# Optimization experiments

Measured on AMD Instinct MI355X. Metric: run time of the kernel, lower is better.

## Reference

```python
import jax, jax.numpy as jnp
import numpy as np

NMS_POST = 500      # nms_post_maxsize
NMS_PRE = 4096      # nms_pre_maxsize
NMS_THRESH = 0.5
SCORE_THRESH = 0.1
NUM_BOXES = 2_000_000
NUM_CLASSES = 10


def setup_inputs() -> dict:
    key = jax.random.key(0)
    k1, k2, k3 = jax.random.split(key, 3)
    # valid axis-aligned boxes: centers in [0,100), sizes in [1,6)
    ctr = jax.random.uniform(k1, (2, NUM_BOXES), dtype=jnp.float32) * 100.0
    wh = 1.0 + jax.random.uniform(k2, (2, NUM_BOXES), dtype=jnp.float32) * 5.0
    x1y1 = ctr - 0.5 * wh
    x2y2 = ctr + 0.5 * wh
    batch_box_preds = jnp.stack([x1y1[0], x1y1[1], x2y2[0], x2y2[1]], axis=0)[None]  # (1,4,N)
    batch_cls_preds = jax.random.uniform(k3, (1, NUM_CLASSES, NUM_BOXES), dtype=jnp.float32)  # (1,C,N)
    return {"batch_box_preds": batch_box_preds, "batch_cls_preds": batch_cls_preds}


def _nms(batch_box_preds, batch_cls_preds):
    boxes = jnp.transpose(batch_box_preds[0])        # (N,4) x1,y1,x2,y2
    cls = batch_cls_preds[0]                          # (C,N)
    scores = jnp.max(cls, axis=0)                     # (N,)
    labels = jnp.argmax(cls, axis=0)                  # (N,) int

    # score threshold: invalidate low scores before top-k
    masked = jnp.where(scores >= SCORE_THRESH, scores, -1.0)
    vals, idx = jax.lax.top_k(masked, NMS_PRE)        # sorted desc
    bk = boxes[idx]                                   # (K,4)
    lk = labels[idx]                                  # (K,)
    valid = vals >= SCORE_THRESH                      # (K,)

    # pairwise IoU (K,K)
    x1, y1, x2, y2 = bk[:, 0], bk[:, 1], bk[:, 2], bk[:, 3]
    area = jnp.clip(x2 - x1, 0.0) * jnp.clip(y2 - y1, 0.0)
    iw = jnp.clip(jnp.minimum(x2[:, None], x2[None, :]) - jnp.maximum(x1[:, None], x1[None, :]), 0.0)
    ih = jnp.clip(jnp.minimum(y2[:, None], y2[None, :]) - jnp.maximum(y1[:, None], y1[None, :]), 0.0)
    inter = iw * ih
    iou = inter / (area[:, None] + area[None, :] - inter + 1e-8)

    # greedy suppression in score order
    K = NMS_PRE
    arange_k = jnp.arange(K)

    def body(keep, i):
        sup = keep[i] & (iou[i] > NMS_THRESH) & (arange_k > i)
        return keep & ~sup, None

    keep, _ = jax.lax.scan(body, valid, arange_k)

    final_scores = jnp.where(keep, vals, -1.0)
    sv, si = jax.lax.top_k(final_scores, NMS_POST)    # top post kept boxes (score order)
    ob = bk[si]                                       # (P,4)
    ol = lk[si]                                       # (P,)
    m = sv >= SCORE_THRESH                            # pad mask
    out = jnp.concatenate(
        [
            jnp.where(m[:, None], ob, 0.0),
            jnp.where(m, sv, 0.0)[:, None],
            jnp.where(m, ol, 0).astype(jnp.float32)[:, None],
        ],
        axis=1,
    )
    return out[None]  # (1, NMS_POST, 6): x1,y1,x2,y2,score,label


def reference(batch_box_preds, batch_cls_preds):
    return _nms(batch_box_preds, batch_cls_preds)
```

## Files before the change

kernel.cpp:

```cpp
#include <hip/hip_runtime.h>
#include <stdint.h>

#define NBOX 2000000
#define NCLS 10
#define KPRE 4096
#define KPOST 500
#define GCAP 6144
#define NMW  (GCAP / 64)
#define PCAP 131072
#define LPC  16384
#define PROWS (GCAP / 64)
#define BSEL 4096

#define OFF_KEYS  ((size_t)0)
#define OFF_PAIRS ((size_t)8000000)
#define OFF_ARR   (OFF_PAIRS + (size_t)PCAP * 4)
#define OFF_LAB   (OFF_ARR + (size_t)GCAP * 32)
#define OFF_ZERO  (OFF_LAB + (size_t)NBOX)
#define ZW_HIST0  0
#define ZW_HIST2  256
#define ZW_HIST16 512
#define ZW_STATE  (512 + 65536)
#define ZERO_WORDS (ZW_STATE + 16)
#define ZERO_BYTES ((size_t)ZERO_WORDS * 4)

#define HOTBASE 0x4080u

__device__ __forceinline__ uint32_t f2ord(float f) {
  uint32_t b = __float_as_uint(f);
  return (b & 0x80000000u) ? ~b : (b | 0x80000000u);
}
__device__ __forceinline__ float ord2f(uint32_t ord) {
  uint32_t b = (ord & 0x80000000u) ? (ord ^ 0x80000000u) : ~ord;
  return __uint_as_float(b);
}

__device__ __forceinline__ unsigned long long shflx64(unsigned long long v, int mask) {
  union { unsigned long long u; int i[2]; } a; a.u = v;
  a.i[0] = __shfl_xor(a.i[0], mask, 64);
  a.i[1] = __shfl_xor(a.i[1], mask, 64);
  return a.u;
}

__device__ __forceinline__ void wave_bucket(const uint32_t* __restrict__ h, uint32_t need,
                                            uint32_t* bin_out, uint32_t* nd_out) {
  int l = threadIdx.x & 63;
  uint4 h4 = reinterpret_cast<const uint4*>(h)[l];
  uint32_t s = h4.x + h4.y + h4.z + h4.w;
  uint32_t p = s;
  #pragma unroll
  for (int d = 1; d < 64; d <<= 1) {
    uint32_t v = __shfl_up(p, d, 64);
    if (l >= d) p += v;
  }
  uint32_t e0 = p - s, e1 = e0 + h4.x, e2 = e1 + h4.y, e3 = e2 + h4.z, e4 = e3 + h4.w;
  uint32_t eb[5] = {e0, e1, e2, e3, e4};
  uint32_t bin = 0xFFFFFFFFu, nd = 1;
  #pragma unroll
  for (int q = 0; q < 4; ++q)
    if (eb[q] < need && need <= eb[q + 1]) { bin = (uint32_t)(4 * l + q); nd = need - eb[q]; }
  unsigned long long mm = __ballot(bin != 0xFFFFFFFFu);
  int src = mm ? __builtin_ctzll(mm) : 0;
  *bin_out = (uint32_t)__shfl((int)bin, src);
  *nd_out  = (uint32_t)__shfl((int)nd, src);
}

__device__ __forceinline__ void wave_compact32(bool take, uint32_t key,
                                               uint32_t* counter, uint32_t* buf,
                                               uint32_t cap) {
  unsigned long long mm = __ballot(take);
  if (take) {
    int lane = threadIdx.x & 63;
    unsigned long long lt = (lane == 0) ? 0ull : (~0ull >> (64 - lane));
    int rank = __builtin_popcountll(mm & lt);
    int leader = __builtin_ctzll(mm);
    uint32_t base = 0;
    if (rank == 0) base = atomicAdd(counter, (uint32_t)__builtin_popcountll(mm));
    base = __shfl(base, leader);
    uint32_t pos = base + (uint32_t)rank;
    if (pos < cap) buf[pos] = key;
  }
}

__device__ __forceinline__ void tree10(float v0, float v1, float v2, float v3, float v4,
                                       float v5, float v6, float v7, float v8, float v9,
                                       float* mv, int* mi) {
  float b0, b1, b2, b3, b4; int j0, j1, j2, j3, j4;
  if (v1 > v0) { b0 = v1; j0 = 1; } else { b0 = v0; j0 = 0; }
  if (v3 > v2) { b1 = v3; j1 = 3; } else { b1 = v2; j1 = 2; }
  if (v5 > v4) { b2 = v5; j2 = 5; } else { b2 = v4; j2 = 4; }
  if (v7 > v6) { b3 = v7; j3 = 7; } else { b3 = v6; j3 = 6; }
  if (v9 > v8) { b4 = v9; j4 = 9; } else { b4 = v8; j4 = 8; }
  if (b1 > b0) { b0 = b1; j0 = j1; }
  if (b3 > b2) { b2 = b3; j2 = j3; }
  if (b2 > b0) { b0 = b2; j0 = j2; }
  if (b4 > b0) { b0 = b4; j0 = j4; }
  *mv = b0; *mi = j0;
}


__global__ void k_score(const float* __restrict__ cls, uint32_t* __restrict__ keys,
                        uint8_t* __restrict__ labs, uint32_t* __restrict__ hist0,
                        uint32_t* __restrict__ hist16) {
  __shared__ uint32_t lh0[256];
  __shared__ uint32_t lhr[128];
  for (int i = threadIdx.x; i < 256; i += blockDim.x) lh0[i] = 0;
  for (int i = threadIdx.x; i < 128; i += blockDim.x) lhr[i] = 0;
  __syncthreads();
  const int nvec = NBOX / 4;
  const float4* cp = reinterpret_cast<const float4*>(cls);
  const int pstr = NBOX / 4;
  for (int v = blockIdx.x * blockDim.x + threadIdx.x; v < nvec; v += gridDim.x * blockDim.x) {
    float4 x0 = cp[v];
    float4 x1 = cp[pstr * 1 + v];
    float4 x2 = cp[pstr * 2 + v];
    float4 x3 = cp[pstr * 3 + v];
    float4 x4 = cp[pstr * 4 + v];
    float4 x5 = cp[pstr * 5 + v];
    float4 x6 = cp[pstr * 6 + v];
    float4 x7 = cp[pstr * 7 + v];
    float4 x8 = cp[pstr * 8 + v];
    float4 x9 = cp[pstr * 9 + v];
    uint32_t u4[4]; int l4[4];
    float mv; int mi;
    tree10(x0.x, x1.x, x2.x, x3.x, x4.x, x5.x, x6.x, x7.x, x8.x, x9.x, &mv, &mi);
    { float ms = (mv >= 0.1f) ? mv : -1.0f; u4[0] = ~f2ord(ms); l4[0] = mi; }
    tree10(x0.y, x1.y, x2.y, x3.y, x4.y, x5.y, x6.y, x7.y, x8.y, x9.y, &mv, &mi);
    { float ms = (mv >= 0.1f) ? mv : -1.0f; u4[1] = ~f2ord(ms); l4[1] = mi; }
    tree10(x0.z, x1.z, x2.z, x3.z, x4.z, x5.z, x6.z, x7.z, x8.z, x9.z, &mv, &mi);
    { float ms = (mv >= 0.1f) ? mv : -1.0f; u4[2] = ~f2ord(ms); l4[2] = mi; }
    tree10(x0.w, x1.w, x2.w, x3.w, x4.w, x5.w, x6.w, x7.w, x8.w, x9.w, &mv, &mi);
    { float ms = (mv >= 0.1f) ? mv : -1.0f; u4[3] = ~f2ord(ms); l4[3] = mi; }
    #pragma unroll
    for (int q = 0; q < 4; ++q) {
      uint32_t b16 = u4[q] >> 16;
      uint32_t rel = b16 - HOTBASE;
      if (rel < 128u) atomicAdd(&lhr[rel], 1u);
      else { atomicAdd(&hist16[b16], 1u); atomicAdd(&lh0[b16 >> 8], 1u); }
    }
    reinterpret_cast<uint4*>(keys)[v] = make_uint4(u4[0], u4[1], u4[2], u4[3]);
    uchar4 lb; lb.x = (uint8_t)l4[0]; lb.y = (uint8_t)l4[1];
    lb.z = (uint8_t)l4[2]; lb.w = (uint8_t)l4[3];
    reinterpret_cast<uchar4*>(labs)[v] = lb;
  }
  __syncthreads();
  for (int i = threadIdx.x; i < 128; i += blockDim.x) {
    uint32_t c = lhr[i];
    if (c) { atomicAdd(&hist16[HOTBASE + i], c); atomicAdd(&lh0[HOTBASE >> 8], c); }
  }
  __syncthreads();
  for (int i = threadIdx.x; i < 256; i += blockDim.x)
    if (lh0[i]) atomicAdd(&hist0[i], lh0[i]);
}

__global__ void k_hist2(const uint32_t* __restrict__ keys,
                        const uint32_t* __restrict__ hist0,
                        const uint32_t* __restrict__ hist16,
                        uint32_t* __restrict__ hist2,
                        float* __restrict__ x1a, float* __restrict__ y1a,
                        float* __restrict__ x2a, float* __restrict__ y2a,
                        float* __restrict__ vala, int* __restrict__ laba,
                        unsigned long long* __restrict__ skg) {
  __shared__ uint32_t lh[256];
  __shared__ uint32_t sp16;
  if (threadIdx.x < 64) {
    uint32_t b1, nd1, b2, nd2;
    wave_bucket(hist0, KPRE, &b1, &nd1);
    wave_bucket(hist16 + ((size_t)b1 << 8), nd1, &b2, &nd2);
    if (threadIdx.x == 0) sp16 = (b1 << 8) | b2;
  }
  for (int i = threadIdx.x; i < 256; i += blockDim.x) lh[i] = 0;
  __syncthreads();
  uint32_t p16 = sp16;
  const int nvec = NBOX / 4;
  int gtid = blockIdx.x * blockDim.x + threadIdx.x;
  int gtot = gridDim.x * blockDim.x;
  for (int v = gtid; v < nvec; v += gtot) {
    uint4 kv = reinterpret_cast<const uint4*>(keys)[v];
    if ((kv.x >> 16) == p16) atomicAdd(&lh[(kv.x >> 8) & 255u], 1u);
    if ((kv.y >> 16) == p16) atomicAdd(&lh[(kv.y >> 8) & 255u], 1u);
    if ((kv.z >> 16) == p16) atomicAdd(&lh[(kv.z >> 8) & 255u], 1u);
    if ((kv.w >> 16) == p16) atomicAdd(&lh[(kv.w >> 8) & 255u], 1u);
  }
  for (int t = gtid; t < GCAP; t += gtot) {
    x1a[t] = 0.0f; y1a[t] = 0.0f; x2a[t] = 0.0f; y2a[t] = 0.0f;
    vala[t] = -1.0f; laba[t] = 0; skg[t] = ~0ull;
  }
  __syncthreads();
  for (int i = threadIdx.x; i < 256; i += blockDim.x)
    if (lh[i]) atomicAdd(&hist2[i], lh[i]);
}

__global__ void k_selgather(const uint32_t* __restrict__ keys,
                            const float* __restrict__ boxes, const uint8_t* __restrict__ labs,
                            const uint32_t* __restrict__ hist0,
                            const uint32_t* __restrict__ hist16,
                            const uint32_t* __restrict__ hist2,
                            uint32_t* __restrict__ selcnt,
                            float* __restrict__ x1a, float* __restrict__ y1a,
                            float* __restrict__ x2a, float* __restrict__ y2a,
                            float* __restrict__ vala, int* __restrict__ laba,
                            unsigned long long* __restrict__ skg) {
  __shared__ uint32_t sp24, bcnt, bbase;
  __shared__ uint32_t lu[BSEL];
  __shared__ uint32_t li[BSEL];
  if (threadIdx.x < 64) {
    uint32_t b1, nd1, b2, nd2, b3, nd3;
    wave_bucket(hist0, KPRE, &b1, &nd1);
    wave_bucket(hist16 + ((size_t)b1 << 8), nd1, &b2, &nd2);
    wave_bucket(hist2, nd2, &b3, &nd3);
    if (threadIdx.x == 0) sp24 = (((b1 << 8) | b2) << 8) | b3;
  }
  if (threadIdx.x == 0) bcnt = 0;
  __syncthreads();
  uint32_t p24 = sp24;
  const int nvec = NBOX / 4;
  for (int v = blockIdx.x * blockDim.x + threadIdx.x; v < nvec; v += gridDim.x * blockDim.x) {
    uint4 kv = reinterpret_cast<const uint4*>(keys)[v];
    uint32_t us[4] = {kv.x, kv.y, kv.z, kv.w};
    #pragma unroll
    for (int q = 0; q < 4; ++q) {
      uint32_t u = us[q];
      if ((u >> 8) <= p24) {
        uint32_t p = atomicAdd(&bcnt, 1u);
        if (p < (uint32_t)BSEL) { lu[p] = u; li[p] = (uint32_t)(4 * v + q); }
      }
    }
  }
  __syncthreads();
  if (threadIdx.x == 0) {
    uint32_t c = bcnt; if (c > (uint32_t)BSEL) c = (uint32_t)BSEL;
    bbase = c ? atomicAdd(selcnt, c) : 0u;
    bcnt = c;
  }
  __syncthreads();
  uint32_t c = bcnt, base = bbase;
  for (uint32_t i = threadIdx.x; i < c; i += blockDim.x) {
    uint32_t pos = base + i;
    if (pos < (uint32_t)GCAP) {
      uint32_t idx = li[i];
      uint32_t u = lu[i];
      x1a[pos] = boxes[idx];
      y1a[pos] = boxes[(size_t)NBOX + idx];
      x2a[pos] = boxes[(size_t)2 * NBOX + idx];
      y2a[pos] = boxes[(size_t)3 * NBOX + idx];
      vala[pos] = ord2f(~u);
      laba[pos] = (int)labs[idx];
      skg[pos] = ((unsigned long long)u << 32) | idx;
    }
  }
}

__global__ void k_pairs(const float* __restrict__ x1a, const float* __restrict__ y1a,
                        const float* __restrict__ x2a, const float* __restrict__ y2a,
                        const unsigned long long* __restrict__ skg,
                        uint32_t* __restrict__ paircnt, uint32_t* __restrict__ pairs) {
#pragma clang fp contract(off)
  int bx = blockIdx.x, by = blockIdx.y;
  if (bx < by) return;
  int t = threadIdx.x;
  int i = by * 64 + t;
  __shared__ float sx1[64], sy1[64], sx2[64], sy2[64], sar[64];
  __shared__ unsigned long long sk[64];
  int j0 = bx * 64 + t;
  float cx1 = x1a[j0], cy1 = y1a[j0], cx2 = x2a[j0], cy2 = y2a[j0];
  sx1[t] = cx1; sy1[t] = cy1; sx2[t] = cx2; sy2[t] = cy2;
  sar[t] = fmaxf(cx2 - cx1, 0.0f) * fmaxf(cy2 - cy1, 0.0f);
  sk[t] = skg[j0];
  __syncthreads();
  float x1i = x1a[i], y1i = y1a[i], x2i = x2a[i], y2i = y2a[i];
  unsigned long long rk = skg[i];
  float ari = fmaxf(x2i - x1i, 0.0f) * fmaxf(y2i - y1i, 0.0f);
  unsigned long long w = 0ull;
  #pragma unroll 8
  for (int jj = 0; jj < 64; ++jj) {
    int j = bx * 64 + jj;
    float iw = fmaxf(fminf(x2i, sx2[jj]) - fmaxf(x1i, sx1[jj]), 0.0f);
    float ih = fmaxf(fminf(y2i, sy2[jj]) - fmaxf(y1i, sy1[jj]), 0.0f);
    float inter = iw * ih;
    float den = ((ari + sar[jj]) - inter) + 1e-8f;
    float iou = inter / den;
    if ((iou > 0.5f) && (j > i)) w |= (1ull << jj);
  }
  while (__ballot(w != 0ull)) {
    bool tk = (w != 0ull);
    uint32_t pr = 0;
    if (tk) {
      int b = __builtin_ctzll(w); w &= w - 1;
      int j = bx * 64 + b;
      bool i_sup = (rk < sk[b]);
      pr = i_sup ? (((uint32_t)i << 16) | (uint32_t)j)
                 : (((uint32_t)j << 16) | (uint32_t)i);
    }
    wave_compact32(tk, pr, paircnt, pairs, (uint32_t)PCAP);
  }
}

__global__ void __launch_bounds__(1024) k_fix(
    const uint32_t* __restrict__ state, const uint32_t* __restrict__ pairs,
    const float* __restrict__ x1a, const float* __restrict__ y1a,
    const float* __restrict__ x2a, const float* __restrict__ y2a,
    const float* __restrict__ vala, const int* __restrict__ laba,
    const unsigned long long* __restrict__ skg, float* __restrict__ out) {
  __shared__ unsigned long long lk[GCAP];
  __shared__ uint32_t lpair[LPC];
  __shared__ unsigned long long validm[NMW], accm[NMW];
  __shared__ uint32_t supp[NMW * 2];
  __shared__ uint32_t hsel[256];
  __shared__ uint32_t lsel[512];
  __shared__ unsigned long long kkbuf[512];
  __shared__ uint32_t chg, scnt2, sneedS;
  __shared__ unsigned long long spre;
  __shared__ uint32_t orlo, orhi, andlo, andhi;
  int tid = threadIdx.x;
  int lane = tid & 63;

  uint32_t gc = state[0]; if (gc > (uint32_t)GCAP) gc = (uint32_t)GCAP;
  uint32_t np = state[1]; if (np > (uint32_t)PCAP) np = (uint32_t)PCAP;
  for (int t = tid; t < KPOST * 6; t += 1024) out[t] = 0.0f;
  if (tid < 512) kkbuf[tid] = ~0ull;
  for (int t = tid; t < GCAP; t += 1024) lk[t] = (t < (int)gc) ? skg[t] : ~0ull;
  bool plds = (np <= (uint32_t)LPC);
  if (plds) for (uint32_t p = (uint32_t)tid; p < np; p += 1024) lpair[p] = pairs[p];
  if (tid == 0) { orlo = 0; orhi = 0; andlo = ~0u; andhi = ~0u; scnt2 = 0; }
  __syncthreads();

  uint32_t need1 = (gc < (uint32_t)KPRE) ? gc : (uint32_t)KPRE;
  if (need1 == 0) return;
  {
    unsigned long long myor = 0ull, myand = ~0ull;
    for (int t = tid; t < (int)gc; t += 1024) {
      unsigned long long k = lk[t];
      myor |= k; myand &= k;
    }
    #pragma unroll
    for (int d = 1; d < 64; d <<= 1) { myor |= shflx64(myor, d); myand &= shflx64(myand, d); }
    if (lane == 0) {
      atomicOr(&orlo, (uint32_t)myor); atomicOr(&orhi, (uint32_t)(myor >> 32));
      atomicAnd(&andlo, (uint32_t)myand); atomicAnd(&andhi, (uint32_t)(myand >> 32));
    }
  }
  __syncthreads();
  unsigned long long T1;
  {
    unsigned long long vor = ((unsigned long long)orhi << 32) | orlo;
    unsigned long long vand = ((unsigned long long)andhi << 32) | andlo;
    unsigned long long diff = vor ^ vand;
    unsigned long long pre = 0;
    uint32_t need = need1;
    for (int b = 7; b >= 0; --b) {
      uint32_t db = (uint32_t)(diff >> (8 * b)) & 255u;
      if (db == 0) { pre = (pre << 8) | ((uint32_t)(vand >> (8 * b)) & 255u); continue; }
      if (tid < 256) hsel[tid] = 0;
      __syncthreads();
      for (int t = tid; t < (int)gc; t += 1024) {
        unsigned long long k = lk[t];
        bool pm = (b == 7) ? true : ((k >> (8 * b + 8)) == pre);
        if (pm) atomicAdd(&hsel[(uint32_t)(k >> (8 * b)) & 255u], 1u);
      }
      __syncthreads();
      if (tid < 64) {
        uint32_t c0 = hsel[4 * tid], c1 = hsel[4 * tid + 1],
                 c2 = hsel[4 * tid + 2], c3 = hsel[4 * tid + 3];
        uint32_t s = c0 + c1 + c2 + c3;
        uint32_t p = s;
        #pragma unroll
        for (int d = 1; d < 64; d <<= 1) {
          uint32_t v = __shfl_up(p, d, 64);
          if (tid >= d) p += v;
        }
        uint32_t e0 = p - s, e1 = e0 + c0, e2 = e1 + c1, e3 = e2 + c2, e4 = e3 + c3;
        uint32_t eb[5] = {e0, e1, e2, e3, e4};
        #pragma unroll
        for (int q = 0; q < 4; ++q)
          if (eb[q] < need && need <= eb[q + 1]) {
            spre = (pre << 8) | (uint32_t)(4 * tid + q);
            sneedS = need - eb[q];
          }
      }
      __syncthreads();
      pre = spre; need = sneedS;
      __syncthreads();
    }
    T1 = pre;
  }

  for (int t = tid; t < GCAP; t += 1024) {
    unsigned long long k = lk[t];
    float v = ord2f(~(uint32_t)(k >> 32));
    bool ok = (k <= T1) && (v >= 0.1f);
    unsigned long long bm = __ballot(ok);
    if (lane == 0) { validm[t >> 6] = bm; accm[t >> 6] = bm; }
  }
  __syncthreads();

  while (true) {
    __syncthreads();
    if (tid < NMW * 2) supp[tid] = 0;
    if (tid == 0) chg = 0;
    __syncthreads();
    if (plds) {
      for (uint32_t p = (uint32_t)tid; p < np; p += 1024) {
        uint32_t pr = lpair[p];
        uint32_t i = pr >> 16, j = pr & 0xffffu;
        if ((accm[i >> 6] >> (i & 63)) & 1ull) atomicOr(&supp[j >> 5], 1u << (j & 31));
      }
    } else {
      for (uint32_t p = (uint32_t)tid; p < np; p += 1024) {
        uint32_t pr = pairs[p];
        uint32_t i = pr >> 16, j = pr & 0xffffu;
        if ((accm[i >> 6] >> (i & 63)) & 1ull) atomicOr(&supp[j >> 5], 1u << (j & 31));
      }
    }
    __syncthreads();
    if (tid < NMW) {
      unsigned long long s = ((unsigned long long)supp[2 * tid + 1] << 32) | supp[2 * tid];
      unsigned long long na = validm[tid] & ~s;
      if (na != accm[tid]) { accm[tid] = na; atomicOr(&chg, 1u); }
    }
    __syncthreads();
    if (chg == 0) break;
  }

  if (tid == 0) {
    uint32_t ns = 0;
    for (int l = 0; l < NMW; ++l) ns += (uint32_t)__builtin_popcountll(accm[l]);
    sneedS = (ns < (uint32_t)KPOST) ? ns : (uint32_t)KPOST;
    orlo = 0; orhi = 0; andlo = ~0u; andhi = ~0u;
  }
  __syncthreads();
  uint32_t need0 = sneedS;
  if (need0 == 0) return;
  {
    unsigned long long myor = 0ull, myand = ~0ull;
    for (int t = tid; t < GCAP; t += 1024) {
      if ((accm[t >> 6] >> (t & 63)) & 1ull) {
        unsigned long long k = lk[t];
        myor |= k; myand &= k;
      }
    }
    #pragma unroll
    for (int d = 1; d < 64; d <<= 1) { myor |= shflx64(myor, d); myand &= shflx64(myand, d); }
    if (lane == 0) {
      atomicOr(&orlo, (uint32_t)myor); atomicOr(&orhi, (uint32_t)(myor >> 32));
      atomicAnd(&andlo, (uint32_t)myand); atomicAnd(&andhi, (uint32_t)(myand >> 32));
    }
  }
  __syncthreads();
  unsigned long long T2;
  {
    unsigned long long vor = ((unsigned long long)orhi << 32) | orlo;
    unsigned long long vand = ((unsigned long long)andhi << 32) | andlo;
    unsigned long long diff = vor ^ vand;
    unsigned long long pre = 0;
    uint32_t need = need0;
    for (int b = 7; b >= 0; --b) {
      uint32_t db = (uint32_t)(diff >> (8 * b)) & 255u;
      if (db == 0) { pre = (pre << 8) | ((uint32_t)(vand >> (8 * b)) & 255u); continue; }
      if (tid < 256) hsel[tid] = 0;
      __syncthreads();
      for (int t = tid; t < GCAP; t += 1024) {
        if ((accm[t >> 6] >> (t & 63)) & 1ull) {
          unsigned long long k = lk[t];
          bool pm = (b == 7) ? true : ((k >> (8 * b + 8)) == pre);
          if (pm) atomicAdd(&hsel[(uint32_t)(k >> (8 * b)) & 255u], 1u);
        }
      }
      __syncthreads();
      if (tid < 64) {
        uint32_t c0 = hsel[4 * tid], c1 = hsel[4 * tid + 1],
                 c2 = hsel[4 * tid + 2], c3 = hsel[4 * tid + 3];
        uint32_t s = c0 + c1 + c2 + c3;
        uint32_t p = s;
        #pragma unroll
        for (int d = 1; d < 64; d <<= 1) {
          uint32_t v = __shfl_up(p, d, 64);
          if (tid >= d) p += v;
        }
        uint32_t e0 = p - s, e1 = e0 + c0, e2 = e1 + c1, e3 = e2 + c2, e4 = e3 + c3;
        uint32_t eb[5] = {e0, e1, e2, e3, e4};
        #pragma unroll
        for (int q = 0; q < 4; ++q)
          if (eb[q] < need && need <= eb[q + 1]) {
            spre = (pre << 8) | (uint32_t)(4 * tid + q);
            sneedS = need - eb[q];
          }
      }
      __syncthreads();
      pre = spre; need = sneedS;
      __syncthreads();
    }
    T2 = pre;
  }

  for (int t = tid; t < GCAP; t += 1024) {
    bool take = ((accm[t >> 6] >> (t & 63)) & 1ull) && (lk[t] <= T2);
    wave_compact32(take, (uint32_t)t, &scnt2, lsel, 512u);
  }
  __syncthreads();
  uint32_t cnt = min(scnt2, 512u);
  if (tid < (int)cnt) kkbuf[tid] = lk[lsel[tid]];
  __syncthreads();
  if (tid < (int)cnt) {
    unsigned long long k0 = kkbuf[tid];
    uint32_t rank = 0;
    #pragma unroll 8
    for (uint32_t p = 0; p < 512u; ++p) rank += (kkbuf[p] < k0) ? 1u : 0u;
    if (rank < (uint32_t)KPOST) {
      int i = (int)lsel[tid];
      out[rank * 6 + 0] = x1a[i];
      out[rank * 6 + 1] = y1a[i];
      out[rank * 6 + 2] = x2a[i];
      out[rank * 6 + 3] = y2a[i];
      out[rank * 6 + 4] = vala[i];
      out[rank * 6 + 5] = (float)laba[i];
    }
  }
}

extern "C" void kernel_launch(void* const* d_in, const int* in_sizes, int n_in,
                              void* d_out, int out_size, void* d_ws, size_t ws_size,
                              hipStream_t stream) {
  const float* boxes = (const float*)d_in[0];
  const float* cls   = (const float*)d_in[1];
  float* out = (float*)d_out;
  char* ws = (char*)d_ws;

  uint32_t* keys = (uint32_t*)(ws + OFF_KEYS);
  uint32_t* pairs = (uint32_t*)(ws + OFF_PAIRS);
  float* x1a = (float*)(ws + OFF_ARR);
  float* y1a = x1a + GCAP;
  float* x2a = y1a + GCAP;
  float* y2a = x2a + GCAP;
  float* vala = y2a + GCAP;
  int* laba = (int*)(vala + GCAP);
  unsigned long long* skg = (unsigned long long*)(laba + GCAP);
  uint8_t* labs = (uint8_t*)(ws + OFF_LAB);
  uint32_t* zbase = (uint32_t*)(ws + OFF_ZERO);
  uint32_t* hist0 = zbase + ZW_HIST0;
  uint32_t* hist2 = zbase + ZW_HIST2;
  uint32_t* hist16 = zbase + ZW_HIST16;
  uint32_t* state = zbase + ZW_STATE;
  uint32_t* selcnt = state;
  uint32_t* paircnt = state + 1;

  hipMemsetAsync(ws + OFF_ZERO, 0, ZERO_BYTES, stream);
  k_score<<<1024, 256, 0, stream>>>(cls, keys, labs, hist0, hist16);
  k_hist2<<<512, 256, 0, stream>>>(keys, hist0, hist16, hist2,
                                   x1a, y1a, x2a, y2a, vala, laba, skg);
  k_selgather<<<512, 256, 0, stream>>>(keys, boxes, labs, hist0, hist16, hist2,
                                       selcnt, x1a, y1a, x2a, y2a, vala, laba, skg);
  k_pairs<<<dim3(PROWS, PROWS), 64, 0, stream>>>(x1a, y1a, x2a, y2a, skg, paircnt, pairs);
  k_fix<<<1, 1024, 0, stream>>>(state, pairs, x1a, y1a, x2a, y2a, vala, laba, skg, out);
}
```

Before: 223.6 us.

## Fuse hist2+selgather and pairs+fix kernels using software grid barriers

Merges the second-level histogram and selection/gather kernels into one persistent 256-block kernel that uses a flag-based grid barrier between the phases. It also merges the pairwise IoU kernel with the single-block fix-up kernel: all blocks compute triangular tiles indexed per wave, then signal block 0, which waits and runs the greedy resolution. The aim is to cut kernel launch gaps and the wasted lower-triangle blocks. The cost is spin-wait barriers that assume all 256 blocks are co-resident, plus a smaller per-block selection buffer.

```diff
diff --git a/kernel.cpp b/kernel.cpp
--- a/kernel.cpp
+++ b/kernel.cpp
@@ -9,8 +9,9 @@
 #define NMW  (GCAP / 64)
 #define PCAP 131072
 #define LPC  16384
-#define PROWS (GCAP / 64)
-#define BSEL 4096
+#define MSEL 2048
+#define NBLKM 256
+#define NWAV 16
 
 #define OFF_KEYS  ((size_t)0)
 #define OFF_PAIRS ((size_t)8000000)
@@ -21,7 +22,10 @@
 #define ZW_HIST2  256
 #define ZW_HIST16 512
 #define ZW_STATE  (512 + 65536)
-#define ZERO_WORDS (ZW_STATE + 16)
+#define SW_REL1   2
+#define SW_FLAGS1 16
+#define SW_FLAGS2 272
+#define ZERO_WORDS (ZW_STATE + 544)
 #define ZERO_BYTES ((size_t)ZERO_WORDS * 4)
 
 #define HOTBASE 0x4080u
@@ -40,6 +44,32 @@
   a.i[0] = __shfl_xor(a.i[0], mask, 64);
   a.i[1] = __shfl_xor(a.i[1], mask, 64);
   return a.u;
+}
+
+__device__ __forceinline__ void mid_bar(uint32_t* flags1, uint32_t* rel1) {
+  __syncthreads();
+  int tid = threadIdx.x;
+  if (blockIdx.x == 0) {
+    if (tid >= 1 && tid < NBLKM) {
+      while (!__hip_atomic_load(&flags1[tid], __ATOMIC_RELAXED, __HIP_MEMORY_SCOPE_AGENT))
+        __builtin_amdgcn_s_sleep(2);
+    }
+    __syncthreads();
+    if (tid == 0) {
+      __threadfence();
+      __hip_atomic_store(rel1, 1u, __ATOMIC_RELAXED, __HIP_MEMORY_SCOPE_AGENT);
+    }
+    __syncthreads();
+  } else {
+    if (tid == 0) {
+      __threadfence();
+      __hip_atomic_store(&flags1[blockIdx.x], 1u, __ATOMIC_RELAXED, __HIP_MEMORY_SCOPE_AGENT);
+      while (!__hip_atomic_load(rel1, __ATOMIC_RELAXED, __HIP_MEMORY_SCOPE_AGENT))
+        __builtin_amdgcn_s_sleep(2);
+      __threadfence();
+    }
+    __syncthreads();
+  }
 }
 
 __device__ __forceinline__ void wave_bucket(const uint32_t* __restrict__ h, uint32_t need,
@@ -153,28 +183,36 @@
     if (lh0[i]) atomicAdd(&hist0[i], lh0[i]);
 }
 
-__global__ void k_hist2(const uint32_t* __restrict__ keys,
-                        const uint32_t* __restrict__ hist0,
-                        const uint32_t* __restrict__ hist16,
-                        uint32_t* __restrict__ hist2,
-                        float* __restrict__ x1a, float* __restrict__ y1a,
-                        float* __restrict__ x2a, float* __restrict__ y2a,
-                        float* __restrict__ vala, int* __restrict__ laba,
-                        unsigned long long* __restrict__ skg) {
+__global__ void __launch_bounds__(1024) k_mid(
+    const uint32_t* __restrict__ keys,
+    const float* __restrict__ boxes, const uint8_t* __restrict__ labs,
+    const uint32_t* __restrict__ hist0, const uint32_t* __restrict__ hist16,
+    uint32_t* __restrict__ hist2, uint32_t* __restrict__ state,
+    float* __restrict__ x1a, float* __restrict__ y1a,
+    float* __restrict__ x2a, float* __restrict__ y2a,
+    float* __restrict__ vala, int* __restrict__ laba,
+    unsigned long long* __restrict__ skg) {
   __shared__ uint32_t lh[256];
-  __shared__ uint32_t sp16;
-  if (threadIdx.x < 64) {
+  __shared__ uint32_t lu[MSEL];
+  __shared__ uint32_t li[MSEL];
+  __shared__ uint32_t sp16, sp24, bcnt, bbase;
+  int tid = threadIdx.x, blk = blockIdx.x;
+  int gtid = blk * 1024 + tid;
+  const int gtot = NBLKM * 1024;
+  const int nvec = NBOX / 4;
+  uint32_t* selcnt = state;
+  uint32_t* flags1 = state + SW_FLAGS1;
+  uint32_t* rel1 = state + SW_REL1;
+
+  if (tid < 64) {
     uint32_t b1, nd1, b2, nd2;
     wave_bucket(hist0, KPRE, &b1, &nd1);
     wave_bucket(hist16 + ((size_t)b1 << 8), nd1, &b2, &nd2);
-    if (threadIdx.x == 0) sp16 = (b1 << 8) | b2;
-  }
-  for (int i = threadIdx.x; i < 256; i += blockDim.x) lh[i] = 0;
+    if (tid == 0) sp16 = (b1 << 8) | b2;
+  }
+  for (int i = tid; i < 256; i += 1024) lh[i] = 0;
   __syncthreads();
   uint32_t p16 = sp16;
-  const int nvec = NBOX / 4;
-  int gtid = blockIdx.x * blockDim.x + threadIdx.x;
-  int gtot = gridDim.x * blockDim.x;
   for (int v = gtid; v < nvec; v += gtot) {
     uint4 kv = reinterpret_cast<const uint4*>(keys)[v];
     if ((kv.x >> 16) == p16) atomicAdd(&lh[(kv.x >> 8) & 255u], 1u);
@@ -187,35 +225,22 @@
     vala[t] = -1.0f; laba[t] = 0; skg[t] = ~0ull;
   }
   __syncthreads();
-  for (int i = threadIdx.x; i < 256; i += blockDim.x)
+  for (int i = tid; i < 256; i += 1024)
     if (lh[i]) atomicAdd(&hist2[i], lh[i]);
-}
-
-__global__ void k_selgather(const uint32_t* __restrict__ keys,
-                            const float* __restrict__ boxes, const uint8_t* __restrict__ labs,
-                            const uint32_t* __restrict__ hist0,
-                            const uint32_t* __restrict__ hist16,
-                            const uint32_t* __restrict__ hist2,
-                            uint32_t* __restrict__ selcnt,
-                            float* __restrict__ x1a, float* __restrict__ y1a,
-                            float* __restrict__ x2a, float* __restrict__ y2a,
-                            float* __restrict__ vala, int* __restrict__ laba,
-                            unsigned long long* __restrict__ skg) {
-  __shared__ uint32_t sp24, bcnt, bbase;
-  __shared__ uint32_t lu[BSEL];
-  __shared__ uint32_t li[BSEL];
-  if (threadIdx.x < 64) {
+
+  mid_bar(flags1, rel1);
+
+  if (tid < 64) {
     uint32_t b1, nd1, b2, nd2, b3, nd3;
     wave_bucket(hist0, KPRE, &b1, &nd1);
     wave_bucket(hist16 + ((size_t)b1 << 8), nd1, &b2, &nd2);
     wave_bucket(hist2, nd2, &b3, &nd3);
-    if (threadIdx.x == 0) sp24 = (((b1 << 8) | b2) << 8) | b3;
-  }
-  if (threadIdx.x == 0) bcnt = 0;
+    if (tid == 0) sp24 = (((b1 << 8) | b2) << 8) | b3;
+  }
+  if (tid == 0) bcnt = 0;
   __syncthreads();
   uint32_t p24 = sp24;
-  const int nvec = NBOX / 4;
-  for (int v = blockIdx.x * blockDim.x + threadIdx.x; v < nvec; v += gridDim.x * blockDim.x) {
+  for (int v = gtid; v < nvec; v += gtot) {
     uint4 kv = reinterpret_cast<const uint4*>(keys)[v];
     uint32_t us[4] = {kv.x, kv.y, kv.z, kv.w};
     #pragma unroll
@@ -223,19 +248,19 @@
       uint32_t u = us[q];
       if ((u >> 8) <= p24) {
         uint32_t p = atomicAdd(&bcnt, 1u);
-        if (p < (uint32_t)BSEL) { lu[p] = u; li[p] = (uint32_t)(4 * v + q); }
-      }
-    }
-  }
-  __syncthreads();
-  if (threadIdx.x == 0) {
-    uint32_t c = bcnt; if (c > (uint32_t)BSEL) c = (uint32_t)BSEL;
+        if (p < (uint32_t)MSEL) { lu[p] = u; li[p] = (uint32_t)(4 * v + q); }
+      }
+    }
+  }
+  __syncthreads();
+  if (tid == 0) {
+    uint32_t c = bcnt; if (c > (uint32_t)MSEL) c = (uint32_t)MSEL;
     bbase = c ? atomicAdd(selcnt, c) : 0u;
     bcnt = c;
   }
   __syncthreads();
   uint32_t c = bcnt, base = bbase;
-  for (uint32_t i = threadIdx.x; i < c; i += blockDim.x) {
+  for (uint32_t i = (uint32_t)tid; i < c; i += 1024) {
     uint32_t pos = base + i;
     if (pos < (uint32_t)GCAP) {
       uint32_t idx = li[i];
@@ -251,57 +276,13 @@
   }
 }
 
-__global__ void k_pairs(const float* __restrict__ x1a, const float* __restrict__ y1a,
-                        const float* __restrict__ x2a, const float* __restrict__ y2a,
-                        const unsigned long long* __restrict__ skg,
-                        uint32_t* __restrict__ paircnt, uint32_t* __restrict__ pairs) {
-#pragma clang fp contract(off)
-  int bx = blockIdx.x, by = blockIdx.y;
-  if (bx < by) return;
-  int t = threadIdx.x;
-  int i = by * 64 + t;
-  __shared__ float sx1[64], sy1[64], sx2[64], sy2[64], sar[64];
-  __shared__ unsigned long long sk[64];
-  int j0 = bx * 64 + t;
-  float cx1 = x1a[j0], cy1 = y1a[j0], cx2 = x2a[j0], cy2 = y2a[j0];
-  sx1[t] = cx1; sy1[t] = cy1; sx2[t] = cx2; sy2[t] = cy2;
-  sar[t] = fmaxf(cx2 - cx1, 0.0f) * fmaxf(cy2 - cy1, 0.0f);
-  sk[t] = skg[j0];
-  __syncthreads();
-  float x1i = x1a[i], y1i = y1a[i], x2i = x2a[i], y2i = y2a[i];
-  unsigned long long rk = skg[i];
-  float ari = fmaxf(x2i - x1i, 0.0f) * fmaxf(y2i - y1i, 0.0f);
-  unsigned long long w = 0ull;
-  #pragma unroll 8
-  for (int jj = 0; jj < 64; ++jj) {
-    int j = bx * 64 + jj;
-    float iw = fmaxf(fminf(x2i, sx2[jj]) - fmaxf(x1i, sx1[jj]), 0.0f);
-    float ih = fmaxf(fminf(y2i, sy2[jj]) - fmaxf(y1i, sy1[jj]), 0.0f);
-    float inter = iw * ih;
-    float den = ((ari + sar[jj]) - inter) + 1e-8f;
-    float iou = inter / den;
-    if ((iou > 0.5f) && (j > i)) w |= (1ull << jj);
-  }
-  while (__ballot(w != 0ull)) {
-    bool tk = (w != 0ull);
-    uint32_t pr = 0;
-    if (tk) {
-      int b = __builtin_ctzll(w); w &= w - 1;
-      int j = bx * 64 + b;
-      bool i_sup = (rk < sk[b]);
-      pr = i_sup ? (((uint32_t)i << 16) | (uint32_t)j)
-                 : (((uint32_t)j << 16) | (uint32_t)i);
-    }
-    wave_compact32(tk, pr, paircnt, pairs, (uint32_t)PCAP);
-  }
-}
-
-__global__ void __launch_bounds__(1024) k_fix(
-    const uint32_t* __restrict__ state, const uint32_t* __restrict__ pairs,
+__global__ void __launch_bounds__(1024) k_tail(
+    uint32_t* __restrict__ state, uint32_t* __restrict__ pairs,
     const float* __restrict__ x1a, const float* __restrict__ y1a,
     const float* __restrict__ x2a, const float* __restrict__ y2a,
     const float* __restrict__ vala, const int* __restrict__ laba,
     const unsigned long long* __restrict__ skg, float* __restrict__ out) {
+#pragma clang fp contract(off)
   __shared__ unsigned long long lk[GCAP];
   __shared__ uint32_t lpair[LPC];
   __shared__ unsigned long long validm[NMW], accm[NMW];
@@ -312,11 +293,89 @@
   __shared__ uint32_t chg, scnt2, sneedS;
   __shared__ unsigned long long spre;
   __shared__ uint32_t orlo, orhi, andlo, andhi;
-  int tid = threadIdx.x;
-  int lane = tid & 63;
+  int tid = threadIdx.x, blk = blockIdx.x;
+  int wid = tid >> 6, lane = tid & 63;
+  uint32_t* paircnt = state + 1;
+  uint32_t* flags2 = state + SW_FLAGS2;
 
   uint32_t gc = state[0]; if (gc > (uint32_t)GCAP) gc = (uint32_t)GCAP;
-  uint32_t np = state[1]; if (np > (uint32_t)PCAP) np = (uint32_t)PCAP;
+
+  {
+    int rows = (int)((gc + 63) >> 6);
+    int NT = rows * (rows + 1) / 2;
+    float* psx1 = (float*)lpair;
+    float* psy1 = psx1 + NWAV * 64;
+    float* psx2 = psy1 + NWAV * 64;
+    float* psy2 = psx2 + NWAV * 64;
+    float* psar = psy2 + NWAV * 64;
+    unsigned long long* psk = (unsigned long long*)(psar + NWAV * 64);
+    int W = blk * NWAV + wid;
+    int wb = wid << 6;
+    for (int T = W; T < NT; T += NBLKM * NWAV) {
+      float Rf = (float)rows;
+      float disc = (2.0f * Rf + 1.0f) * (2.0f * Rf + 1.0f) - 8.0f * (float)T;
+      disc = disc > 0.0f ? disc : 0.0f;
+      int by = (int)(((2.0f * Rf + 1.0f) - sqrtf(disc)) * 0.5f);
+      if (by < 0) by = 0;
+      if (by > rows - 1) by = rows - 1;
+      while (by > 0 && T < by * rows - (by * (by - 1)) / 2) --by;
+      while (by < rows - 1 && T >= (by + 1) * rows - ((by + 1) * by) / 2) ++by;
+      int cum = by * rows - (by * (by - 1)) / 2;
+      int bx = by + (T - cum);
+      int i = by * 64 + lane;
+      int j0 = bx * 64 + lane;
+      float cx1 = x1a[j0], cy1 = y1a[j0], cx2 = x2a[j0], cy2 = y2a[j0];
+      psx1[wb + lane] = cx1; psy1[wb + lane] = cy1;
+      psx2[wb + lane] = cx2; psy2[wb + lane] = cy2;
+      psar[wb + lane] = fmaxf(cx2 - cx1, 0.0f) * fmaxf(cy2 - cy1, 0.0f);
+      psk[wb + lane] = skg[j0];
+      float x1i = x1a[i], y1i = y1a[i], x2i = x2a[i], y2i = y2a[i];
+      unsigned long long rk = skg[i];
+      float ari = fmaxf(x2i - x1i, 0.0f) * fmaxf(y2i - y1i, 0.0f);
+      unsigned long long w = 0ull;
+      #pragma unroll 8
+      for (int jj = 0; jj < 64; ++jj) {
+        int j = bx * 64 + jj;
+        float iw = fmaxf(fminf(x2i, psx2[wb + jj]) - fmaxf(x1i, psx1[wb + jj]), 0.0f);
+        float ih = fmaxf(fminf(y2i, psy2[wb + jj]) - fmaxf(y1i, psy1[wb + jj]), 0.0f);
+        float inter = iw * ih;
+        float den = ((ari + psar[wb + jj]) - inter) + 1e-8f;
+        float iou = inter / den;
+        if ((iou > 0.5f) && (j > i)) w |= (1ull << jj);
+      }
+      while (__ballot(w != 0ull)) {
+        bool tk = (w != 0ull);
+        uint32_t pr = 0;
+        if (tk) {
+          int b = __builtin_ctzll(w); w &= w - 1;
+          int j = bx * 64 + b;
+          bool i_sup = (rk < psk[wb + b]);
+          pr = i_sup ? (((uint32_t)i << 16) | (uint32_t)j)
+                     : (((uint32_t)j << 16) | (uint32_t)i);
+        }
+        wave_compact32(tk, pr, paircnt, pairs, (uint32_t)PCAP);
+      }
+    }
+  }
+
+  __syncthreads();
+  if (blk != 0) {
+    if (tid == 0) {
+      __threadfence();
+      __hip_atomic_store(&flags2[blk], 1u, __ATOMIC_RELAXED, __HIP_MEMORY_SCOPE_AGENT);
+    }
+    return;
+  }
+  if (tid >= 1 && tid < NBLKM) {
+    while (!__hip_atomic_load(&flags2[tid], __ATOMIC_RELAXED, __HIP_MEMORY_SCOPE_AGENT))
+      __builtin_amdgcn_s_sleep(2);
+  }
+  __syncthreads();
+  if (tid == 0) __threadfence();
+  __syncthreads();
+
+  uint32_t np = __hip_atomic_load(paircnt, __ATOMIC_RELAXED, __HIP_MEMORY_SCOPE_AGENT);
+  if (np > (uint32_t)PCAP) np = (uint32_t)PCAP;
   for (int t = tid; t < KPOST * 6; t += 1024) out[t] = 0.0f;
   if (tid < 512) kkbuf[tid] = ~0ull;
   for (int t = tid; t < GCAP; t += 1024) lk[t] = (t < (int)gc) ? skg[t] : ~0ull;
@@ -541,15 +600,11 @@
   uint32_t* hist2 = zbase + ZW_HIST2;
   uint32_t* hist16 = zbase + ZW_HIST16;
   uint32_t* state = zbase + ZW_STATE;
-  uint32_t* selcnt = state;
-  uint32_t* paircnt = state + 1;
 
   hipMemsetAsync(ws + OFF_ZERO, 0, ZERO_BYTES, stream);
   k_score<<<1024, 256, 0, stream>>>(cls, keys, labs, hist0, hist16);
-  k_hist2<<<512, 256, 0, stream>>>(keys, hist0, hist16, hist2,
-                                   x1a, y1a, x2a, y2a, vala, laba, skg);
-  k_selgather<<<512, 256, 0, stream>>>(keys, boxes, labs, hist0, hist16, hist2,
-                                       selcnt, x1a, y1a, x2a, y2a, vala, laba, skg);
-  k_pairs<<<dim3(PROWS, PROWS), 64, 0, stream>>>(x1a, y1a, x2a, y2a, skg, paircnt, pairs);
-  k_fix<<<1, 1024, 0, stream>>>(state, pairs, x1a, y1a, x2a, y2a, vala, laba, skg, out);
-}
+  k_mid<<<NBLKM, 1024, 0, stream>>>(keys, boxes, labs, hist0, hist16, hist2, state,
+                                    x1a, y1a, x2a, y2a, vala, laba, skg);
+  k_tail<<<NBLKM, 1024, 0, stream>>>(state, pairs, x1a, y1a, x2a, y2a,
+                                     vala, laba, skg, out);
+}
```

Measured after the change: 218.6 us. 1.02x faster.
